# Performance work log

Hardware: AMD Instinct MI355X
Metric: run time of the kernel (lower is better)

## Reference

```python
import jax, jax.numpy as jnp
import numpy as np

N, E = 50000, 600000
IN, H, C = 128, 8, 32
HC = H * C
LAT, OUT, NCOM = 32, 64, 30
BN_EPS = 1e-5
NEG_SLOPE = 0.2


def setup_inputs() -> dict:
    key = jax.random.key(0)
    ks = jax.random.split(key, 32)
    f32 = jnp.float32
    def rn(i, shape, s=0.05):
        return jax.random.normal(ks[i], shape, f32) * s
    inp = {
        'x': jax.random.normal(ks[0], (N, IN), f32),
        'eps': jax.random.normal(ks[1], (N, LAT), f32),
        'edge_index': jax.random.randint(ks[2], (2, E), 0, N, jnp.int32),
        # GAT layer 1 (in -> H*C)
        'gat1_W': rn(3, (IN, HC)), 'gat1_asrc': rn(4, (H, C)), 'gat1_adst': rn(5, (H, C)), 'gat1_b': jnp.zeros((HC,), f32),
        'bn1_g': jnp.ones((HC,), f32), 'bn1_b': jnp.zeros((HC,), f32),
        # GAT layer 2 (H*C -> H*C)
        'gat2_W': rn(6, (HC, HC)), 'gat2_asrc': rn(7, (H, C)), 'gat2_adst': rn(8, (H, C)), 'gat2_b': jnp.zeros((HC,), f32),
        'bn2_g': jnp.ones((HC,), f32), 'bn2_b': jnp.zeros((HC,), f32),
        # GAT layer 3 (H*C -> H*C)
        'gat3_W': rn(9, (HC, HC)), 'gat3_asrc': rn(10, (H, C)), 'gat3_adst': rn(11, (H, C)), 'gat3_b': jnp.zeros((HC,), f32),
        'bn3_g': jnp.ones((HC,), f32), 'bn3_b': jnp.zeros((HC,), f32),
        # heads
        'res_W': rn(12, (IN, HC)), 'res_b': jnp.zeros((HC,), f32),
        'mu_W': rn(13, (HC, LAT)), 'mu_b': jnp.zeros((LAT,), f32),
        'lv_W': rn(14, (HC, LAT)), 'lv_b': jnp.zeros((LAT,), f32),
        'dec_W': rn(15, (LAT, OUT)), 'dec_b': jnp.zeros((OUT,), f32),
        'aux_W': rn(16, (HC, NCOM)), 'aux_b': jnp.zeros((NCOM,), f32),
    }
    return inp


def gat_conv(x, src, dst, W, asrc, adst, b):
    # PyG GATConv (concat=True, self-loops already in src/dst, lin bias=False)
    n = x.shape[0]
    h = (x @ W).reshape(n, H, C)                      # [N,H,C]
    a_s = jnp.einsum('nhc,hc->nh', h, asrc)           # [N,H]
    a_d = jnp.einsum('nhc,hc->nh', h, adst)
    e = jax.nn.leaky_relu(a_s[src] + a_d[dst], NEG_SLOPE)  # [E,H]
    m = jax.ops.segment_max(e, dst, num_segments=n)        # per-dest softmax (stable)
    p = jnp.exp(e - m[dst])
    s = jax.ops.segment_sum(p, dst, num_segments=n)
    alpha = p / (s[dst] + 1e-16)                      # [E,H]
    out = jax.ops.segment_sum(h[src] * alpha[:, :, None], dst, num_segments=n)
    return out.reshape(n, HC) + b


def batch_norm(x, g, b):
    mu = x.mean(0)
    var = x.var(0)  # biased var, as torch BN uses for normalization
    return (x - mu) * jax.lax.rsqrt(var + BN_EPS) * g + b


def reference(x, eps, edge_index,
              gat1_W, gat1_asrc, gat1_adst, gat1_b, bn1_g, bn1_b,
              gat2_W, gat2_asrc, gat2_adst, gat2_b, bn2_g, bn2_b,
              gat3_W, gat3_asrc, gat3_adst, gat3_b, bn3_g, bn3_b,
              res_W, res_b, mu_W, mu_b, lv_W, lv_b, dec_W, dec_b, aux_W, aux_b):
    loops = jnp.arange(N, dtype=edge_index.dtype)
    src = jnp.concatenate([edge_index[0], loops])
    dst = jnp.concatenate([edge_index[1], loops])

    residual = x @ res_W + res_b
    h = jax.nn.relu(batch_norm(gat_conv(x, src, dst, gat1_W, gat1_asrc, gat1_adst, gat1_b), bn1_g, bn1_b))
    h = jax.nn.relu(batch_norm(gat_conv(h, src, dst, gat2_W, gat2_asrc, gat2_adst, gat2_b), bn2_g, bn2_b))
    h = jax.nn.relu(batch_norm(gat_conv(h, src, dst, gat3_W, gat3_asrc, gat3_adst, gat3_b), bn3_g, bn3_b))
    h = h + residual

    mu = h @ mu_W + mu_b
    logvar = h @ lv_W + lv_b
    z = mu + eps * jnp.exp(0.5 * logvar)   # reparameterize
    out = z @ dec_W + dec_b
    aux = h @ aux_W + aux_b
    return (out, mu, logvar, aux)
```

## Files before the change

### kernel.cpp

```cpp
#include <hip/hip_runtime.h>

#define N_NODES 50000
#define N_EDGES 600000
#define HC 256
#define NH 8
#define AGG_BLOCKS 2048
#define AGG_WAVES (AGG_BLOCKS * 4)

typedef short s8v __attribute__((ext_vector_type(8)));
typedef float f4v __attribute__((ext_vector_type(4)));
typedef _Float16 h4v __attribute__((ext_vector_type(4)));
typedef __attribute__((address_space(1))) const unsigned int as1_cu32;
typedef __attribute__((address_space(3))) unsigned int as3_u32;

__device__ inline ushort f2bf(float f) {
  unsigned u = __float_as_uint(f);
  unsigned r = u + 0x7FFF + ((u >> 16) & 1);
  return (ushort)(r >> 16);
}

__global__ void k_init_cnt(int* __restrict__ cnt) {
  int i = blockIdx.x * 256 + threadIdx.x;
  if (i < N_NODES) cnt[i] = 1;
}

__global__ void k_count(const int* __restrict__ dstE, int* __restrict__ cnt) {
  int e = blockIdx.x * 256 + threadIdx.x;
  if (e < N_EDGES) atomicAdd(&cnt[dstE[e]], 1);
}

__global__ void k_scan_bsum(const int* __restrict__ cnt, int* __restrict__ bsum) {
  __shared__ int sd[256];
  int i = blockIdx.x * 256 + threadIdx.x;
  sd[threadIdx.x] = (i < N_NODES) ? cnt[i] : 0;
  __syncthreads();
  for (int o = 128; o > 0; o >>= 1) {
    if (threadIdx.x < o) sd[threadIdx.x] += sd[threadIdx.x + o];
    __syncthreads();
  }
  if (threadIdx.x == 0) bsum[blockIdx.x] = sd[0];
}

__global__ void k_scan_offsets(int* __restrict__ bsum, int nb) {
  __shared__ int s[256];
  int t = threadIdx.x;
  int v = (t < nb) ? bsum[t] : 0;
  s[t] = v; __syncthreads();
  for (int o = 1; o < 256; o <<= 1) {
    int x = (t >= o) ? s[t - o] : 0;
    __syncthreads();
    s[t] += x;
    __syncthreads();
  }
  if (t < nb) bsum[t] = s[t] - v;
}

__global__ void k_scan_write(const int* __restrict__ cnt, const int* __restrict__ bsum,
                             int* __restrict__ rowptr, int* __restrict__ fillptr) {
  __shared__ int s[256];
  int t = threadIdx.x;
  int i = blockIdx.x * 256 + t;
  int v = (i < N_NODES) ? cnt[i] : 0;
  s[t] = v; __syncthreads();
  for (int o = 1; o < 256; o <<= 1) {
    int x = (t >= o) ? s[t - o] : 0;
    __syncthreads();
    s[t] += x;
    __syncthreads();
  }
  int excl = s[t] - v + bsum[blockIdx.x];
  if (i < N_NODES) {
    rowptr[i] = excl;
    fillptr[i] = excl;
    if (i == N_NODES - 1) rowptr[N_NODES] = excl + v;
  }
}

__global__ void k_fill(const int* __restrict__ srcE, const int* __restrict__ dstE,
                       int* __restrict__ fillptr, int* __restrict__ srcs) {
  int i = blockIdx.x * 256 + threadIdx.x;
  if (i < N_NODES) {
    int pos = atomicAdd(&fillptr[i], 1);
    srcs[pos] = i;
  } else if (i < N_NODES + N_EDGES) {
    int e = i - N_NODES;
    int pos = atomicAdd(&fillptr[dstE[e]], 1);
    srcs[pos] = srcE[e];
  }
}

__global__ void k_cvt_x(const float* __restrict__ X, ushort* __restrict__ Xb) {
  size_t i = ((size_t)blockIdx.x * 256 + threadIdx.x) * 4;
  float4 x4 = *(const float4*)&X[i];
  ushort4 o;
  o.x = f2bf(x4.x); o.y = f2bf(x4.y); o.z = f2bf(x4.z); o.w = f2bf(x4.w);
  *(ushort4*)&Xb[i] = o;
}

__global__ void k_cvt_wt(const float* __restrict__ W, ushort* __restrict__ Wt, int K, int Nw) {
  __shared__ ushort s[32][33];
  int tx = threadIdx.x & 31, ty = threadIdx.x >> 5;
  int k0 = blockIdx.x * 32, n0 = blockIdx.y * 32;
  for (int j = 0; j < 32; j += 8)
    s[ty + j][tx] = f2bf(W[(size_t)(k0 + ty + j) * Nw + n0 + tx]);
  __syncthreads();
  for (int j = 0; j < 32; j += 8)
    Wt[(size_t)(n0 + ty + j) * K + k0 + tx] = s[tx][ty + j];
}

__global__ void k_pack_head(const float* __restrict__ muW, const float* __restrict__ lvW,
                            const float* __restrict__ auxW, ushort* __restrict__ Wth) {
  int n = blockIdx.x;
  int k = threadIdx.x;
  float v = 0.f;
  if (n < 32) v = muW[k * 32 + n];
  else if (n < 64) v = lvW[k * 32 + (n - 32)];
  else if (n < 94) v = auxW[k * 30 + (n - 64)];
  Wth[n * 256 + k] = f2bf(v);
}

template <typename OutT>
__launch_bounds__(256)
__global__ void k_gemm_bf16(const ushort* __restrict__ A, const ushort* __restrict__ Wt,
                            const float* __restrict__ bias, OutT* __restrict__ Out,
                            int M, int K, int ldc) {
  __shared__ __align__(16) ushort As[16 * 512];
  __shared__ __align__(16) ushort Bs[16 * 512];
  int t = threadIdx.x, w = t >> 6, L = t & 63;
  int bm = blockIdx.x * 128, bn = blockIdx.y * 128;
  int lrow = L & 15, lcol = (L >> 4) * 8;

  const ushort* ga[4];
  const ushort* gb[4];
#pragma unroll
  for (int u = 0; u < 4; u++) {
    int i = w * 4 + u;
    int mt = i >> 1, ks = i & 1;
    int arow = bm + mt * 16 + lrow;
    if (arow >= M) arow = M - 1;
    ga[u] = A + (size_t)arow * K + ks * 32 + lcol;
    int brow = bn + mt * 16 + lrow;
    gb[u] = Wt + (size_t)brow * K + ks * 32 + lcol;
  }

  f4v acc[4][4];
  f4v zero = {0.f, 0.f, 0.f, 0.f};
#pragma unroll
  for (int mi = 0; mi < 4; mi++)
#pragma unroll
    for (int ni = 0; ni < 4; ni++) acc[mi][ni] = zero;

  int wm = (w >> 1) * 4;
  int wn = (w & 1) * 4;

  int nk = K >> 6;
  for (int kt = 0; kt < nk; kt++) {
#pragma unroll
    for (int u = 0; u < 4; u++) {
      int i = w * 4 + u;
      __builtin_amdgcn_global_load_lds((as1_cu32*)ga[u], (as3_u32*)&As[i * 512], 16, 0, 0);
      __builtin_amdgcn_global_load_lds((as1_cu32*)gb[u], (as3_u32*)&Bs[i * 512], 16, 0, 0);
      ga[u] += 64; gb[u] += 64;
    }
    __syncthreads();
#pragma unroll
    for (int ks = 0; ks < 2; ks++) {
      s8v af[4], bf[4];
#pragma unroll
      for (int mi = 0; mi < 4; mi++)
        af[mi] = *(const s8v*)&As[(((wm + mi) * 2 + ks) * 64 + L) * 8];
#pragma unroll
      for (int ni = 0; ni < 4; ni++)
        bf[ni] = *(const s8v*)&Bs[(((wn + ni) * 2 + ks) * 64 + L) * 8];
#pragma unroll
      for (int mi = 0; mi < 4; mi++)
#pragma unroll
        for (int ni = 0; ni < 4; ni++)
          acc[mi][ni] = __builtin_amdgcn_mfma_f32_16x16x32_bf16(af[mi], bf[ni], acc[mi][ni], 0, 0, 0);
    }
    __syncthreads();
  }
#pragma unroll
  for (int ni = 0; ni < 4; ni++) {
    int col = bn + (wn + ni) * 16 + (L & 15);
    float bb = bias ? bias[col] : 0.f;
#pragma unroll
    for (int mi = 0; mi < 4; mi++) {
      int rbase = bm + (wm + mi) * 16 + (L >> 4) * 4;
#pragma unroll
      for (int i = 0; i < 4; i++) {
        int r = rbase + i;
        if (r < M) Out[(size_t)r * ldc + col] = (OutT)(acc[mi][ni][i] + bb);
      }
    }
  }
}

__launch_bounds__(256)
__global__ void k_att(const _Float16* __restrict__ B, const float* __restrict__ asrc,
                      const float* __restrict__ adst,
                      float* __restrict__ as_, float* __restrict__ ad_) {
  int wid = (blockIdx.x * 256 + threadIdx.x) >> 6;
  int lane = threadIdx.x & 63;
  h4v x = *(const h4v*)&B[(size_t)wid * 256 + (lane << 2)];
  float4 s4 = *(const float4*)&asrc[lane << 2];
  float4 d4 = *(const float4*)&adst[lane << 2];
  float x0 = (float)x[0], x1 = (float)x[1], x2 = (float)x[2], x3 = (float)x[3];
  float vs = x0 * s4.x + x1 * s4.y + x2 * s4.z + x3 * s4.w;
  float vd = x0 * d4.x + x1 * d4.y + x2 * d4.z + x3 * d4.w;
  vs += __shfl_xor(vs, 1); vs += __shfl_xor(vs, 2); vs += __shfl_xor(vs, 4);
  vd += __shfl_xor(vd, 1); vd += __shfl_xor(vd, 2); vd += __shfl_xor(vd, 4);
  if ((lane & 7) == 0) {
    as_[wid * NH + (lane >> 3)] = vs;
    ad_[wid * NH + (lane >> 3)] = vd;
  }
}

__launch_bounds__(256)
__global__ void k_agg(const int* __restrict__ rowptr, const int* __restrict__ srcs,
                      const float* __restrict__ as_, const float* __restrict__ ad_,
                      const _Float16* __restrict__ B, const float* __restrict__ gb,
                      _Float16* __restrict__ C, float* __restrict__ part,
                      float* __restrict__ stats) {
  __shared__ float ss[4 * 512];
  int t = threadIdx.x;
  if (blockIdx.x == 0) {
    stats[t] = 0.f; stats[t + 256] = 0.f;
  }
  int w = t >> 6, lane = t & 63;
  int h = lane >> 3;
  int cb = lane << 2;
  float4 g4 = *(const float4*)&gb[cb];
  float sts0 = 0.f, sts1 = 0.f, sts2 = 0.f, sts3 = 0.f;
  float stq0 = 0.f, stq1 = 0.f, stq2 = 0.f, stq3 = 0.f;

  for (int n = blockIdx.x * 4 + w; n < N_NODES; n += AGG_WAVES) {
    int beg = rowptr[n], end = rowptr[n + 1];
    float ad_nh = ad_[n * NH + h];
    float ac0 = 0.f, ac1 = 0.f, ac2 = 0.f, ac3 = 0.f, wsum = 0.f;
    int k = beg;
    for (; k + 4 <= end; k += 4) {
      int s0 = srcs[k], s1 = srcs[k + 1], s2 = srcs[k + 2], s3 = srcs[k + 3];
      h4v b0 = *(const h4v*)&B[(size_t)s0 * 256 + cb];
      h4v b1 = *(const h4v*)&B[(size_t)s1 * 256 + cb];
      h4v b2 = *(const h4v*)&B[(size_t)s2 * 256 + cb];
      h4v b3 = *(const h4v*)&B[(size_t)s3 * 256 + cb];
      float e0 = as_[s0 * NH + h] + ad_nh; e0 = e0 > 0.f ? e0 : 0.2f * e0;
      float e1 = as_[s1 * NH + h] + ad_nh; e1 = e1 > 0.f ? e1 : 0.2f * e1;
      float e2 = as_[s2 * NH + h] + ad_nh; e2 = e2 > 0.f ? e2 : 0.2f * e2;
      float e3 = as_[s3 * NH + h] + ad_nh; e3 = e3 > 0.f ? e3 : 0.2f * e3;
      float p0 = __expf(e0), p1 = __expf(e1), p2 = __expf(e2), p3 = __expf(e3);
      wsum += (p0 + p1) + (p2 + p3);
      ac0 += p0 * (float)b0[0] + p1 * (float)b1[0] + p2 * (float)b2[0] + p3 * (float)b3[0];
      ac1 += p0 * (float)b0[1] + p1 * (float)b1[1] + p2 * (float)b2[1] + p3 * (float)b3[1];
      ac2 += p0 * (float)b0[2] + p1 * (float)b1[2] + p2 * (float)b2[2] + p3 * (float)b3[2];
      ac3 += p0 * (float)b0[3] + p1 * (float)b1[3] + p2 * (float)b2[3] + p3 * (float)b3[3];
    }
    for (; k < end; k++) {
      int s = srcs[k];
      h4v b4 = *(const h4v*)&B[(size_t)s * 256 + cb];
      float e = as_[s * NH + h] + ad_nh;
      e = e > 0.f ? e : 0.2f * e;
      float p = __expf(e);
      wsum += p;
      ac0 += p * (float)b4[0]; ac1 += p * (float)b4[1];
      ac2 += p * (float)b4[2]; ac3 += p * (float)b4[3];
    }
    float inv = 1.f / (wsum + 1e-16f);
    float v0 = ac0 * inv + g4.x, v1 = ac1 * inv + g4.y;
    float v2 = ac2 * inv + g4.z, v3 = ac3 * inv + g4.w;
    h4v o; o[0] = (_Float16)v0; o[1] = (_Float16)v1; o[2] = (_Float16)v2; o[3] = (_Float16)v3;
    *(h4v*)&C[(size_t)n * 256 + cb] = o;
    sts0 += v0; stq0 += v0 * v0;
    sts1 += v1; stq1 += v1 * v1;
    sts2 += v2; stq2 += v2 * v2;
    sts3 += v3; stq3 += v3 * v3;
  }
  float* sw = &ss[w * 512];
  sw[cb + 0] = sts0; sw[cb + 1] = sts1; sw[cb + 2] = sts2; sw[cb + 3] = sts3;
  sw[256 + cb + 0] = stq0; sw[256 + cb + 1] = stq1;
  sw[256 + cb + 2] = stq2; sw[256 + cb + 3] = stq3;
  __syncthreads();
  float p0 = ss[t] + ss[512 + t] + ss[1024 + t] + ss[1536 + t];
  float p1 = ss[256 + t] + ss[768 + t] + ss[1280 + t] + ss[1792 + t];
  part[(size_t)blockIdx.x * 512 + t] = p0;
  part[(size_t)blockIdx.x * 512 + 256 + t] = p1;
}

__global__ void k_bn_reduce(const float* __restrict__ part, float* __restrict__ stats) {
  int i = threadIdx.x;
  int base = blockIdx.x * (AGG_BLOCKS / 16);
  float s0 = 0.f, s1 = 0.f;
  for (int b = 0; b < AGG_BLOCKS / 16; b++) {
    s0 += part[(size_t)(base + b) * 512 + i];
    s1 += part[(size_t)(base + b) * 512 + 256 + i];
  }
  atomicAdd(&stats[i], s0);
  atomicAdd(&stats[256 + i], s1);
}

__global__ void k_bn_relu_cvt(const _Float16* __restrict__ X, const float* __restrict__ stats,
                              const float* __restrict__ g, const float* __restrict__ b,
                              const _Float16* __restrict__ resid, ushort* __restrict__ Xb) {
  size_t i = ((size_t)blockIdx.x * 256 + threadIdx.x) * 4;
  int c = (int)(i & 255);
  const float invN = 1.f / (float)N_NODES;
  h4v x4 = *(const h4v*)&X[i];
  float4 s4 = *(const float4*)&stats[c];
  float4 q4 = *(const float4*)&stats[256 + c];
  float4 g4 = *(const float4*)&g[c];
  float4 b4 = *(const float4*)&b[c];
  float m0 = s4.x * invN, m1 = s4.y * invN, m2 = s4.z * invN, m3 = s4.w * invN;
  float v0 = ((float)x4[0] - m0) * rsqrtf(q4.x * invN - m0 * m0 + 1e-5f) * g4.x + b4.x;
  float v1 = ((float)x4[1] - m1) * rsqrtf(q4.y * invN - m1 * m1 + 1e-5f) * g4.y + b4.y;
  float v2 = ((float)x4[2] - m2) * rsqrtf(q4.z * invN - m2 * m2 + 1e-5f) * g4.z + b4.z;
  float v3 = ((float)x4[3] - m3) * rsqrtf(q4.w * invN - m3 * m3 + 1e-5f) * g4.w + b4.w;
  v0 = v0 > 0.f ? v0 : 0.f; v1 = v1 > 0.f ? v1 : 0.f;
  v2 = v2 > 0.f ? v2 : 0.f; v3 = v3 > 0.f ? v3 : 0.f;
  if (resid) {
    h4v r4 = *(const h4v*)&resid[i];
    v0 += (float)r4[0]; v1 += (float)r4[1]; v2 += (float)r4[2]; v3 += (float)r4[3];
  }
  ushort4 ob;
  ob.x = f2bf(v0); ob.y = f2bf(v1); ob.z = f2bf(v2); ob.w = f2bf(v3);
  *(ushort4*)&Xb[i] = ob;
}

__launch_bounds__(256)
__global__ void k_dec(const _Float16* __restrict__ Hd, const float* __restrict__ eps,
                      const float* __restrict__ mub, const float* __restrict__ lvb,
                      const float* __restrict__ auxb,
                      const float* __restrict__ decW, const float* __restrict__ decb,
                      float* __restrict__ out) {
  __shared__ float wsd[2048];
  __shared__ float shz[4][32];
  int t = threadIdx.x;
  for (int i = t; i < 2048; i += 256) wsd[i] = decW[i];
  int w = t >> 6, lane = t & 63;
  int n = blockIdx.x * 4 + w;
  const _Float16* hd = &Hd[(size_t)n * 128];
  if (lane < 32) {
    float mu = (float)hd[lane] + mub[lane];
    float lv = (float)hd[32 + lane] + lvb[lane];
    out[(size_t)N_NODES * 64 + (size_t)n * 32 + lane] = mu;
    out[(size_t)N_NODES * 96 + (size_t)n * 32 + lane] = lv;
    shz[w][lane] = mu + eps[(size_t)n * 32 + lane] * __expf(0.5f * lv);
  } else if (lane < 62) {
    int j = lane - 32;
    out[(size_t)N_NODES * 128 + (size_t)n * 30 + j] = (float)hd[64 + j] + auxb[j];
  }
  __syncthreads();
  float o = decb[lane];
#pragma unroll 8
  for (int k = 0; k < 32; k++) o += shz[w][k] * wsd[k * 64 + lane];
  out[(size_t)n * 64 + lane] = o;
}

extern "C" void kernel_launch(void* const* d_in, const int* in_sizes, int n_in,
                              void* d_out, int out_size, void* d_ws, size_t ws_size,
                              hipStream_t stream) {
  (void)in_sizes; (void)n_in; (void)out_size; (void)ws_size;
  const float* x    = (const float*)d_in[0];
  const float* eps  = (const float*)d_in[1];
  const int*   ei   = (const int*)d_in[2];
  const float* gW[3]    = {(const float*)d_in[3],  (const float*)d_in[9],  (const float*)d_in[15]};
  const float* gasrc[3] = {(const float*)d_in[4],  (const float*)d_in[10], (const float*)d_in[16]};
  const float* gadst[3] = {(const float*)d_in[5],  (const float*)d_in[11], (const float*)d_in[17]};
  const float* gbias[3] = {(const float*)d_in[6],  (const float*)d_in[12], (const float*)d_in[18]};
  const float* bng[3]   = {(const float*)d_in[7],  (const float*)d_in[13], (const float*)d_in[19]};
  const float* bnb[3]   = {(const float*)d_in[8],  (const float*)d_in[14], (const float*)d_in[20]};
  const float* resW = (const float*)d_in[21];
  const float* resb = (const float*)d_in[22];
  const float* muW  = (const float*)d_in[23];
  const float* mub  = (const float*)d_in[24];
  const float* lvW  = (const float*)d_in[25];
  const float* lvb  = (const float*)d_in[26];
  const float* decW = (const float*)d_in[27];
  const float* decb = (const float*)d_in[28];
  const float* auxW = (const float*)d_in[29];
  const float* auxb = (const float*)d_in[30];
  float* out = (float*)d_out;

  char* ws = (char*)d_ws;
  size_t off = 0;
  auto alloc = [&](size_t bytes) -> void* {
    void* p = ws + off;
    off += (bytes + 255) & ~(size_t)255;
    return p;
  };
  _Float16* X0  = (_Float16*)alloc((size_t)N_NODES * HC * 2);
  _Float16* X1  = (_Float16*)alloc((size_t)N_NODES * HC * 2);
  _Float16* Rr  = (_Float16*)alloc((size_t)N_NODES * HC * 2);
  _Float16* Hd  = (_Float16*)alloc((size_t)N_NODES * 128 * 2);
  ushort* Xb    = (ushort*)alloc((size_t)N_NODES * HC * 2);
  float*  as_   = (float*)alloc((size_t)N_NODES * NH * 4);
  float*  ad_   = (float*)alloc((size_t)N_NODES * NH * 4);
  float*  stats = (float*)alloc(512 * 4);
  float*  part  = (float*)alloc((size_t)AGG_BLOCKS * 512 * 4);
  int* cnt      = (int*)alloc((size_t)N_NODES * 4);
  int* rowptr   = (int*)alloc((size_t)(N_NODES + 1) * 4);
  int* fillptr  = (int*)alloc((size_t)N_NODES * 4);
  int* srcs     = (int*)alloc((size_t)(N_NODES + N_EDGES) * 4);
  int* bsum     = (int*)alloc(256 * 4);
  ushort* Wt1   = (ushort*)alloc(256 * 128 * 2);
  ushort* Wt2   = (ushort*)alloc(256 * 256 * 2);
  ushort* Wt3   = (ushort*)alloc(256 * 256 * 2);
  ushort* WtR   = (ushort*)alloc(256 * 128 * 2);
  ushort* Wth   = (ushort*)alloc(128 * 256 * 2);

  const int NB = (N_NODES + 255) / 256;
  k_init_cnt<<<NB, 256, 0, stream>>>(cnt);
  k_count<<<(N_EDGES + 255) / 256, 256, 0, stream>>>(ei + N_EDGES, cnt);
  k_scan_bsum<<<NB, 256, 0, stream>>>(cnt, bsum);
  k_scan_offsets<<<1, 256, 0, stream>>>(bsum, NB);
  k_scan_write<<<NB, 256, 0, stream>>>(cnt, bsum, rowptr, fillptr);
  k_fill<<<(N_NODES + N_EDGES + 255) / 256, 256, 0, stream>>>(ei, ei + N_EDGES, fillptr, srcs);

  k_cvt_wt<<<dim3(4, 8), 256, 0, stream>>>(gW[0], Wt1, 128, 256);
  k_cvt_wt<<<dim3(8, 8), 256, 0, stream>>>(gW[1], Wt2, 256, 256);
  k_cvt_wt<<<dim3(8, 8), 256, 0, stream>>>(gW[2], Wt3, 256, 256);
  k_cvt_wt<<<dim3(4, 8), 256, 0, stream>>>(resW, WtR, 128, 256);
  k_pack_head<<<128, 256, 0, stream>>>(muW, lvW, auxW, Wth);
  k_cvt_x<<<(N_NODES * 128) / 1024, 256, 0, stream>>>(x, Xb);

  const int GM = (N_NODES + 127) / 128;
  k_gemm_bf16<_Float16><<<dim3(GM, 2), 256, 0, stream>>>(Xb, WtR, resb, Rr, N_NODES, 128, 256);

  const ushort* Wts[3] = {Wt1, Wt2, Wt3};
  int K = 128;
  for (int L = 0; L < 3; L++) {
    k_gemm_bf16<_Float16><<<dim3(GM, 2), 256, 0, stream>>>(Xb, Wts[L], nullptr, X0, N_NODES, K, 256);
    k_att<<<N_NODES / 4, 256, 0, stream>>>(X0, gasrc[L], gadst[L], as_, ad_);
    k_agg<<<AGG_BLOCKS, 256, 0, stream>>>(rowptr, srcs, as_, ad_, X0, gbias[L], X1, part, stats);
    k_bn_reduce<<<16, 256, 0, stream>>>(part, stats);
    k_bn_relu_cvt<<<(N_NODES * HC) / 1024, 256, 0, stream>>>(
        X1, stats, bng[L], bnb[L], (L == 2) ? Rr : nullptr, Xb);
    K = 256;
  }
  k_gemm_bf16<_Float16><<<dim3(GM, 1), 256, 0, stream>>>(Xb, Wth, nullptr, Hd, N_NODES, 256, 128);
  k_dec<<<N_NODES / 4, 256, 0, stream>>>(Hd, eps, mub, lvb, auxb, decW, decb, out);
}
```

Measured before the change: 651.9 us.

## Fuse attention logits into GEMM epilogue, merge residual GEMM, use fp16 packed aggregation

Computes per-head source/destination attention scores inside the GEMM epilogue via cross-lane reductions and atomics, removing the separate attention kernel and its reread of the projected features. The residual projection is folded into the layer-1 GEMM launch as extra grid columns. The aggregation loop switches to packed half-precision accumulation to halve arithmetic work. The score buffers are zeroed in existing kernels. This adds atomic traffic and risks precision loss or overflow from fp16 accumulation of unnormalized exponentials.

```diff
diff --git a/kernel.cpp b/kernel.cpp
--- a/kernel.cpp
+++ b/kernel.cpp
@@ -6,10 +6,12 @@
 #define NH 8
 #define AGG_BLOCKS 2048
 #define AGG_WAVES (AGG_BLOCKS * 4)
+#define ASD_N (N_NODES * NH * 2)
 
 typedef short s8v __attribute__((ext_vector_type(8)));
 typedef float f4v __attribute__((ext_vector_type(4)));
 typedef _Float16 h4v __attribute__((ext_vector_type(4)));
+typedef _Float16 h2v __attribute__((ext_vector_type(2)));
 typedef __attribute__((address_space(1))) const unsigned int as1_cu32;
 typedef __attribute__((address_space(3))) unsigned int as3_u32;
 
@@ -89,8 +91,11 @@
   }
 }
 
-__global__ void k_cvt_x(const float* __restrict__ X, ushort* __restrict__ Xb) {
-  size_t i = ((size_t)blockIdx.x * 256 + threadIdx.x) * 4;
+__global__ void k_cvt_x(const float* __restrict__ X, ushort* __restrict__ Xb,
+                        float* __restrict__ asd) {
+  int gid = blockIdx.x * 256 + threadIdx.x;
+  if (gid < ASD_N) asd[gid] = 0.f;
+  size_t i = (size_t)gid * 4;
   float4 x4 = *(const float4*)&X[i];
   ushort4 o;
   o.x = f2bf(x4.x); o.y = f2bf(x4.y); o.z = f2bf(x4.z); o.w = f2bf(x4.w);
@@ -119,15 +124,29 @@
   Wth[n * 256 + k] = f2bf(v);
 }
 
-template <typename OutT>
+template <typename OutT, bool ATT, bool RES>
 __launch_bounds__(256)
 __global__ void k_gemm_bf16(const ushort* __restrict__ A, const ushort* __restrict__ Wt,
                             const float* __restrict__ bias, OutT* __restrict__ Out,
-                            int M, int K, int ldc) {
+                            int M, int K, int ldc,
+                            const float* __restrict__ asrcf, const float* __restrict__ adstf,
+                            float* __restrict__ as_g, float* __restrict__ ad_g,
+                            const ushort* __restrict__ Wt2, const float* __restrict__ bias2,
+                            OutT* __restrict__ Out2) {
   __shared__ __align__(16) ushort As[16 * 512];
   __shared__ __align__(16) ushort Bs[16 * 512];
   int t = threadIdx.x, w = t >> 6, L = t & 63;
-  int bm = blockIdx.x * 128, bn = blockIdx.y * 128;
+  int bm = blockIdx.x * 128;
+  int bn = blockIdx.y * 128;
+  const ushort* Wsel = Wt;
+  const float* bsel = bias;
+  OutT* Osel = Out;
+  bool doatt = ATT;
+  if (RES && blockIdx.y >= 2) {
+    Wsel = Wt2; bsel = bias2; Osel = Out2;
+    bn = (blockIdx.y - 2) * 128;
+    doatt = false;
+  }
   int lrow = L & 15, lcol = (L >> 4) * 8;
 
   const ushort* ga[4];
@@ -140,7 +159,7 @@
     if (arow >= M) arow = M - 1;
     ga[u] = A + (size_t)arow * K + ks * 32 + lcol;
     int brow = bn + mt * 16 + lrow;
-    gb[u] = Wt + (size_t)brow * K + ks * 32 + lcol;
+    gb[u] = Wsel + (size_t)brow * K + ks * 32 + lcol;
   }
 
   f4v acc[4][4];
@@ -183,36 +202,49 @@
 #pragma unroll
   for (int ni = 0; ni < 4; ni++) {
     int col = bn + (wn + ni) * 16 + (L & 15);
-    float bb = bias ? bias[col] : 0.f;
+    float bb = bsel ? bsel[col] : 0.f;
 #pragma unroll
     for (int mi = 0; mi < 4; mi++) {
       int rbase = bm + (wm + mi) * 16 + (L >> 4) * 4;
 #pragma unroll
       for (int i = 0; i < 4; i++) {
         int r = rbase + i;
-        if (r < M) Out[(size_t)r * ldc + col] = (OutT)(acc[mi][ni][i] + bb);
+        if (r < M) Osel[(size_t)r * ldc + col] = (OutT)(acc[mi][ni][i] + bb);
       }
     }
   }
-}
-
-__launch_bounds__(256)
-__global__ void k_att(const _Float16* __restrict__ B, const float* __restrict__ asrc,
-                      const float* __restrict__ adst,
-                      float* __restrict__ as_, float* __restrict__ ad_) {
-  int wid = (blockIdx.x * 256 + threadIdx.x) >> 6;
-  int lane = threadIdx.x & 63;
-  h4v x = *(const h4v*)&B[(size_t)wid * 256 + (lane << 2)];
-  float4 s4 = *(const float4*)&asrc[lane << 2];
-  float4 d4 = *(const float4*)&adst[lane << 2];
-  float x0 = (float)x[0], x1 = (float)x[1], x2 = (float)x[2], x3 = (float)x[3];
-  float vs = x0 * s4.x + x1 * s4.y + x2 * s4.z + x3 * s4.w;
-  float vd = x0 * d4.x + x1 * d4.y + x2 * d4.z + x3 * d4.w;
-  vs += __shfl_xor(vs, 1); vs += __shfl_xor(vs, 2); vs += __shfl_xor(vs, 4);
-  vd += __shfl_xor(vd, 1); vd += __shfl_xor(vd, 2); vd += __shfl_xor(vd, 4);
-  if ((lane & 7) == 0) {
-    as_[wid * NH + (lane >> 3)] = vs;
-    ad_[wid * NH + (lane >> 3)] = vd;
+  if (ATT && doatt) {
+    int l = L & 15, q = L >> 4;
+    int base = bn + wn * 16;
+    int h0 = base >> 5;
+    float sa0 = asrcf[base + l],      sa1 = asrcf[base + 16 + l];
+    float sa2 = asrcf[base + 32 + l], sa3 = asrcf[base + 48 + l];
+    float da0 = adstf[base + l],      da1 = adstf[base + 16 + l];
+    float da2 = adstf[base + 32 + l], da3 = adstf[base + 48 + l];
+#pragma unroll
+    for (int mi = 0; mi < 4; mi++) {
+#pragma unroll
+      for (int i = 0; i < 4; i++) {
+        float pas0 = acc[mi][0][i] * sa0 + acc[mi][1][i] * sa1;
+        float pas1 = acc[mi][2][i] * sa2 + acc[mi][3][i] * sa3;
+        float pad0 = acc[mi][0][i] * da0 + acc[mi][1][i] * da1;
+        float pad1 = acc[mi][2][i] * da2 + acc[mi][3][i] * da3;
+#pragma unroll
+        for (int o = 1; o <= 8; o <<= 1) {
+          pas0 += __shfl_xor(pas0, o); pas1 += __shfl_xor(pas1, o);
+          pad0 += __shfl_xor(pad0, o); pad1 += __shfl_xor(pad1, o);
+        }
+        if (l == 0) {
+          int r = bm + (wm + mi) * 16 + q * 4 + i;
+          if (r < M) {
+            atomicAdd(&as_g[r * NH + h0], pas0);
+            atomicAdd(&as_g[r * NH + h0 + 1], pas1);
+            atomicAdd(&ad_g[r * NH + h0], pad0);
+            atomicAdd(&ad_g[r * NH + h0 + 1], pad1);
+          }
+        }
+      }
+    }
   }
 }
 
@@ -237,7 +269,9 @@
   for (int n = blockIdx.x * 4 + w; n < N_NODES; n += AGG_WAVES) {
     int beg = rowptr[n], end = rowptr[n + 1];
     float ad_nh = ad_[n * NH + h];
-    float ac0 = 0.f, ac1 = 0.f, ac2 = 0.f, ac3 = 0.f, wsum = 0.f;
+    h2v a01 = {(_Float16)0, (_Float16)0};
+    h2v a23 = {(_Float16)0, (_Float16)0};
+    float wsum = 0.f;
     int k = beg;
     for (; k + 4 <= end; k += 4) {
       int s0 = srcs[k], s1 = srcs[k + 1], s2 = srcs[k + 2], s3 = srcs[k + 3];
@@ -251,10 +285,14 @@
       float e3 = as_[s3 * NH + h] + ad_nh; e3 = e3 > 0.f ? e3 : 0.2f * e3;
       float p0 = __expf(e0), p1 = __expf(e1), p2 = __expf(e2), p3 = __expf(e3);
       wsum += (p0 + p1) + (p2 + p3);
-      ac0 += p0 * (float)b0[0] + p1 * (float)b1[0] + p2 * (float)b2[0] + p3 * (float)b3[0];
-      ac1 += p0 * (float)b0[1] + p1 * (float)b1[1] + p2 * (float)b2[1] + p3 * (float)b3[1];
-      ac2 += p0 * (float)b0[2] + p1 * (float)b1[2] + p2 * (float)b2[2] + p3 * (float)b3[2];
-      ac3 += p0 * (float)b0[3] + p1 * (float)b1[3] + p2 * (float)b2[3] + p3 * (float)b3[3];
+      _Float16 q0 = (_Float16)p0, q1 = (_Float16)p1, q2 = (_Float16)p2, q3 = (_Float16)p3;
+      h2v pp0 = {q0, q0}, pp1 = {q1, q1}, pp2 = {q2, q2}, pp3 = {q3, q3};
+      h2v b0l = __builtin_shufflevector(b0, b0, 0, 1), b0h = __builtin_shufflevector(b0, b0, 2, 3);
+      h2v b1l = __builtin_shufflevector(b1, b1, 0, 1), b1h = __builtin_shufflevector(b1, b1, 2, 3);
+      h2v b2l = __builtin_shufflevector(b2, b2, 0, 1), b2h = __builtin_shufflevector(b2, b2, 2, 3);
+      h2v b3l = __builtin_shufflevector(b3, b3, 0, 1), b3h = __builtin_shufflevector(b3, b3, 2, 3);
+      a01 += pp0 * b0l + pp1 * b1l + pp2 * b2l + pp3 * b3l;
+      a23 += pp0 * b0h + pp1 * b1h + pp2 * b2h + pp3 * b3h;
     }
     for (; k < end; k++) {
       int s = srcs[k];
@@ -263,12 +301,14 @@
       e = e > 0.f ? e : 0.2f * e;
       float p = __expf(e);
       wsum += p;
-      ac0 += p * (float)b4[0]; ac1 += p * (float)b4[1];
-      ac2 += p * (float)b4[2]; ac3 += p * (float)b4[3];
+      _Float16 qq = (_Float16)p;
+      h2v pp = {qq, qq};
+      a01 += pp * __builtin_shufflevector(b4, b4, 0, 1);
+      a23 += pp * __builtin_shufflevector(b4, b4, 2, 3);
     }
     float inv = 1.f / (wsum + 1e-16f);
-    float v0 = ac0 * inv + g4.x, v1 = ac1 * inv + g4.y;
-    float v2 = ac2 * inv + g4.z, v3 = ac3 * inv + g4.w;
+    float v0 = (float)a01[0] * inv + g4.x, v1 = (float)a01[1] * inv + g4.y;
+    float v2 = (float)a23[0] * inv + g4.z, v3 = (float)a23[1] * inv + g4.w;
     h4v o; o[0] = (_Float16)v0; o[1] = (_Float16)v1; o[2] = (_Float16)v2; o[3] = (_Float16)v3;
     *(h4v*)&C[(size_t)n * 256 + cb] = o;
     sts0 += v0; stq0 += v0 * v0;
@@ -287,16 +327,18 @@
   part[(size_t)blockIdx.x * 512 + 256 + t] = p1;
 }
 
-__global__ void k_bn_reduce(const float* __restrict__ part, float* __restrict__ stats) {
+__global__ void k_bn_reduce(const float* __restrict__ part, float* __restrict__ stats,
+                            float* __restrict__ asd) {
   int i = threadIdx.x;
-  int base = blockIdx.x * (AGG_BLOCKS / 16);
+  int base = blockIdx.x * (AGG_BLOCKS / 128);
   float s0 = 0.f, s1 = 0.f;
-  for (int b = 0; b < AGG_BLOCKS / 16; b++) {
+  for (int b = 0; b < AGG_BLOCKS / 128; b++) {
     s0 += part[(size_t)(base + b) * 512 + i];
     s1 += part[(size_t)(base + b) * 512 + 256 + i];
   }
   atomicAdd(&stats[i], s0);
   atomicAdd(&stats[256 + i], s1);
+  for (int z = blockIdx.x * 256 + i; z < ASD_N; z += 128 * 256) asd[z] = 0.f;
 }
 
 __global__ void k_bn_relu_cvt(const _Float16* __restrict__ X, const float* __restrict__ stats,
@@ -393,8 +435,9 @@
   _Float16* Rr  = (_Float16*)alloc((size_t)N_NODES * HC * 2);
   _Float16* Hd  = (_Float16*)alloc((size_t)N_NODES * 128 * 2);
   ushort* Xb    = (ushort*)alloc((size_t)N_NODES * HC * 2);
-  float*  as_   = (float*)alloc((size_t)N_NODES * NH * 4);
-  float*  ad_   = (float*)alloc((size_t)N_NODES * NH * 4);
+  float*  asd   = (float*)alloc((size_t)ASD_N * 4);
+  float*  as_   = asd;
+  float*  ad_   = asd + (size_t)N_NODES * NH;
   float*  stats = (float*)alloc(512 * 4);
   float*  part  = (float*)alloc((size_t)AGG_BLOCKS * 512 * 4);
   int* cnt      = (int*)alloc((size_t)N_NODES * 4);
@@ -421,22 +464,29 @@
   k_cvt_wt<<<dim3(8, 8), 256, 0, stream>>>(gW[2], Wt3, 256, 256);
   k_cvt_wt<<<dim3(4, 8), 256, 0, stream>>>(resW, WtR, 128, 256);
   k_pack_head<<<128, 256, 0, stream>>>(muW, lvW, auxW, Wth);
-  k_cvt_x<<<(N_NODES * 128) / 1024, 256, 0, stream>>>(x, Xb);
+  k_cvt_x<<<(N_NODES * 128) / 1024, 256, 0, stream>>>(x, Xb, asd);
 
   const int GM = (N_NODES + 127) / 128;
-  k_gemm_bf16<_Float16><<<dim3(GM, 2), 256, 0, stream>>>(Xb, WtR, resb, Rr, N_NODES, 128, 256);
-
   const ushort* Wts[3] = {Wt1, Wt2, Wt3};
   int K = 128;
   for (int L = 0; L < 3; L++) {
-    k_gemm_bf16<_Float16><<<dim3(GM, 2), 256, 0, stream>>>(Xb, Wts[L], nullptr, X0, N_NODES, K, 256);
-    k_att<<<N_NODES / 4, 256, 0, stream>>>(X0, gasrc[L], gadst[L], as_, ad_);
+    if (L == 0) {
+      k_gemm_bf16<_Float16, true, true><<<dim3(GM, 4), 256, 0, stream>>>(
+          Xb, Wts[0], nullptr, X0, N_NODES, K, 256,
+          gasrc[0], gadst[0], as_, ad_, WtR, resb, Rr);
+    } else {
+      k_gemm_bf16<_Float16, true, false><<<dim3(GM, 2), 256, 0, stream>>>(
+          Xb, Wts[L], nullptr, X0, N_NODES, K, 256,
+          gasrc[L], gadst[L], as_, ad_, nullptr, nullptr, nullptr);
+    }
     k_agg<<<AGG_BLOCKS, 256, 0, stream>>>(rowptr, srcs, as_, ad_, X0, gbias[L], X1, part, stats);
-    k_bn_reduce<<<16, 256, 0, stream>>>(part, stats);
+    k_bn_reduce<<<128, 256, 0, stream>>>(part, stats, asd);
     k_bn_relu_cvt<<<(N_NODES * HC) / 1024, 256, 0, stream>>>(
         X1, stats, bng[L], bnb[L], (L == 2) ? Rr : nullptr, Xb);
     K = 256;
   }
-  k_gemm_bf16<_Float16><<<dim3(GM, 1), 256, 0, stream>>>(Xb, Wth, nullptr, Hd, N_NODES, 256, 128);
+  k_gemm_bf16<_Float16, false, false><<<dim3(GM, 1), 256, 0, stream>>>(
+      Xb, Wth, nullptr, Hd, N_NODES, 256, 128,
+      nullptr, nullptr, nullptr, nullptr, nullptr, nullptr, nullptr);
   k_dec<<<N_NODES / 4, 256, 0, stream>>>(Hd, eps, mub, lvb, auxb, decW, decb, out);
 }
```

Measured after the change: 722.1 us. 10.8% more time.
